# Performance work log

Hardware: AMD Instinct MI355X
Metric: run time of the kernel (lower is better)

The kernel has to match this reference:

```python
import jax, jax.numpy as jnp
import numpy as np

N, E, G = 100000, 3200000, 5000
EPS = 1e-5
HEADS, HC = 8, 16


def setup_inputs() -> dict:
    key = jax.random.key(0)
    k = jax.random.split(key, 12)

    def lin(kk, fi, fo):
        return (jax.random.normal(kk, (fi, fo), jnp.float32) / np.sqrt(fi)).astype(jnp.float32)

    return {
        "x": jax.random.normal(k[0], (N, 20), jnp.float32),
        "edge_index": jax.random.randint(k[1], (2, E), 0, N, dtype=jnp.int32),
        "batch": jnp.sort(jax.random.randint(k[2], (N,), 0, G, dtype=jnp.int32)),
        "W1": lin(k[3], 20, 64), "b1": jnp.zeros((64,), jnp.float32),
        "g1": jnp.ones((64,), jnp.float32), "be1": jnp.zeros((64,), jnp.float32),
        "W2": lin(k[4], 64, 32), "b2": jnp.zeros((32,), jnp.float32),
        "g2": jnp.ones((32,), jnp.float32), "be2": jnp.zeros((32,), jnp.float32),
        "W3": lin(k[5], 32, 16), "b3": jnp.zeros((16,), jnp.float32),
        "g3": jnp.ones((16,), jnp.float32), "be3": jnp.zeros((16,), jnp.float32),
        "Wg": lin(k[6], 16, HEADS * HC),
        "att_src": jax.random.normal(k[7], (HEADS, HC), jnp.float32) * 0.1,
        "att_dst": jax.random.normal(k[8], (HEADS, HC), jnp.float32) * 0.1,
        "bg": jnp.zeros((HC,), jnp.float32),
        "Wf": lin(k[9], 16, 3), "bf": jnp.zeros((3,), jnp.float32),
    }


def reference(x, edge_index, batch,
              W1, b1, g1, be1, W2, b2, g2, be2, W3, b3, g3, be3,
              Wg, att_src, att_dst, bg, Wf, bf):
    src, dst = edge_index[0], edge_index[1]
    loop = jnp.arange(N, dtype=src.dtype)
    src_sl = jnp.concatenate([src, loop])  # self-loops (GCN + GAT add_self_loops)
    dst_sl = jnp.concatenate([dst, loop])

    # GCN symmetric normalization D^-1/2 (A+I) D^-1/2
    deg = jax.ops.segment_sum(jnp.ones_like(src_sl, dtype=jnp.float32), dst_sl, N)
    dinv = jnp.where(deg > 0, 1.0 / jnp.sqrt(deg), 0.0)
    norm = (dinv[src_sl] * dinv[dst_sl])[:, None]  # [E+N, 1]

    def gcn(h, W, b):
        h = h @ W
        return jax.ops.segment_sum(h[src_sl] * norm, dst_sl, N) + b

    def bn_relu(h, g, b):  # BatchNorm1d (train-mode batch stats) + ReLU
        mu = h.mean(0)
        var = ((h - mu) ** 2).mean(0)
        return jax.nn.relu(g * (h - mu) * jax.lax.rsqrt(var + EPS) + b)

    h = bn_relu(gcn(x, W1, b1), g1, be1)   # dropout = identity (eval)
    h = bn_relu(gcn(h, W2, b2), g2, be2)
    h = bn_relu(gcn(h, W3, b3), g3, be3)

    # GATConv: heads=8, concat=False (mean over heads), eval -> no dropout
    xg = (h @ Wg).reshape(N, HEADS, HC)
    a_src = (xg * att_src).sum(-1)  # [N, H]
    a_dst = (xg * att_dst).sum(-1)
    logit = jax.nn.leaky_relu(a_src[src_sl] + a_dst[dst_sl], 0.2)  # [E+N, H]
    m = jax.ops.segment_max(logit, dst_sl, N)          # segment softmax over dst
    e = jnp.exp(logit - m[dst_sl])
    s = jax.ops.segment_sum(e, dst_sl, N)
    alpha = e / s[dst_sl]
    agg = jax.ops.segment_sum(xg[src_sl] * alpha[:, :, None], dst_sl, N)  # [N,H,C]
    hg = agg.mean(1) + bg  # [N, 16]

    pooled = jax.ops.segment_sum(hg, batch, G)  # global_add_pool -> [G, 16]
    return pooled @ Wf + bf  # [G, 3]
```

## Files before the change

### kernel.cpp

```cpp
#include <hip/hip_runtime.h>
#include <hip/hip_fp16.h>

constexpr int NN = 100000;
constexpr int EE = 3200000;
constexpr int GG = 5000;
constexpr float BNEPS = 1e-5f;

constexpr int BINS = 128;
constexpr int NPB = (NN + BINS - 1) / BINS;
constexpr int BCHUNK = 8192;
constexpr int NBCH = (EE + BCHUNK - 1) / BCHUNK;
constexpr int BINCAP2 = 96;
constexpr int BINREG = 27648;
constexpr int LCAP = 26624;
constexpr int CTR_STRIDE = 32;

typedef int int4v __attribute__((ext_vector_type(4)));


__global__ __launch_bounds__(1024) void bin_edges(const int* __restrict__ ei,
                                                  uint2* __restrict__ pairs,
                                                  int* __restrict__ binCur) {
    __shared__ int bcnt[BINS];
    __shared__ int bbase[BINS];
    __shared__ uint2 buf[BINS][BINCAP2];
    const int t = threadIdx.x;
    const int lane = t & 63, wv = t >> 6;
    for (int ch = blockIdx.x; ch < NBCH; ch += gridDim.x) {
        for (int k = t; k < BINS; k += 1024) bcnt[k] = 0;
        __syncthreads();
        const int qbase = ch * (BCHUNK / 4);
#pragma unroll
        for (int rep = 0; rep < 2; ++rep) {
            const int q = qbase + rep * 1024 + t;
            if (q < EE / 4) {
                int4v d = __builtin_nontemporal_load((const int4v*)(ei + EE) + q);
                int4v s = __builtin_nontemporal_load((const int4v*)ei + q);
                int dd[4] = {d.x, d.y, d.z, d.w};
                int ss[4] = {s.x, s.y, s.z, s.w};
#pragma unroll
                for (int k = 0; k < 4; ++k) {
                    int o = dd[k] / NPB;
                    int p = atomicAdd(&bcnt[o], 1);
                    if (p < BINCAP2) {
                        buf[o][p] = make_uint2((unsigned)dd[k], (unsigned)ss[k]);
                    } else {
                        int gp = atomicAdd(&binCur[o * CTR_STRIDE], 1);
                        pairs[(size_t)o * BINREG + gp] =
                            make_uint2((unsigned)dd[k], (unsigned)ss[k]);
                    }
                }
            }
        }
        __syncthreads();
        if (t < BINS) {
            int c = bcnt[t] < BINCAP2 ? bcnt[t] : BINCAP2;
            bbase[t] = atomicAdd(&binCur[t * CTR_STRIDE], c);
            bcnt[t] = c;
        }
        __syncthreads();
        for (int o = wv; o < BINS; o += 16) {
            const int c = bcnt[o];
            const size_t base = (size_t)o * BINREG + bbase[o];
            for (int k = lane; k < c; k += 64) pairs[base + k] = buf[o][k];
        }
        __syncthreads();
    }
}


__global__ void bin_base(const int* __restrict__ binCur, int* __restrict__ binBase) {
    __shared__ int s[BINS];
    const int t = threadIdx.x;
    const int v = binCur[t * CTR_STRIDE];
    s[t] = v;
    __syncthreads();
    for (int off = 1; off < BINS; off <<= 1) {
        int add = (t >= off) ? s[t - off] : 0;
        __syncthreads();
        s[t] += add;
        __syncthreads();
    }
    binBase[t] = s[t] - v;
}


__global__ __launch_bounds__(1024) void scatter_lds(const uint2* __restrict__ pairs,
                                                    const int* __restrict__ binCur,
                                                    const int* __restrict__ binBase,
                                                    int* __restrict__ rowptr,
                                                    float* __restrict__ dinv,
                                                    int* __restrict__ colA) {
    __shared__ int scnt[NPB];
    __shared__ int sscan[1024];
    __shared__ int lbuf[LCAP];
    const int b = blockIdx.x;
    const int t = threadIdx.x;
    const int lo = b * NPB;
    const int hi = (lo + NPB < NN) ? lo + NPB : NN;
    const int nb = hi - lo;
    const int tot = binCur[b * CTR_STRIDE];
    const int base = binBase[b];
    const uint2* p = pairs + (size_t)b * BINREG;
    for (int k = t; k < nb; k += 1024) scnt[k] = 0;
    __syncthreads();
    for (int q = t; q < tot; q += 1024) atomicAdd(&scnt[p[q].x - lo], 1);
    __syncthreads();
    const int myc = (t < nb) ? scnt[t] : 0;
    sscan[t] = myc;
    __syncthreads();
    for (int off = 1; off < 1024; off <<= 1) {
        int add = (t >= off) ? sscan[t - off] : 0;
        __syncthreads();
        sscan[t] += add;
        __syncthreads();
    }
    const int excl = sscan[t] - myc;
    if (t < nb) {
        rowptr[lo + t] = base + excl;
        dinv[lo + t] = rsqrtf((float)(myc + 1));
        scnt[t] = excl;
    }
    if (b == BINS - 1 && t == 0) rowptr[NN] = base + tot;
    __syncthreads();
    for (int q = t; q < tot; q += 1024) {
        uint2 e = p[q];
        int pos = atomicAdd(&scnt[e.x - lo], 1);
        if (pos < LCAP) lbuf[pos] = (int)e.y;
        else colA[base + pos] = (int)e.y;
    }
    __syncthreads();
    const int m = tot < LCAP ? tot : LCAP;
    for (int k = t; k < m; k += 1024) colA[base + k] = lbuf[k];
}


__global__ void scale_x(const float* __restrict__ x, const float* __restrict__ dinv,
                        __half* __restrict__ xsc) {
    int idx = blockIdx.x * blockDim.x + threadIdx.x;
    if (idx < NN * 20) {
        int n = idx / 20;
        xsc[idx] = __float2half(x[idx] * dinv[n]);
    }
}


template <int FIN, int FOUT, bool AFFINE, bool SCALED, bool STATS>
__global__ void gemm_k(const float* __restrict__ hin,
                       const float* __restrict__ sumsIn, const float* __restrict__ ssqIn,
                       const float* __restrict__ g, const float* __restrict__ be,
                       const float* __restrict__ W, const float* __restrict__ dinv,
                       const float* __restrict__ bias,
                       float* __restrict__ outF, __half* __restrict__ outH,
                       float* __restrict__ sumsOut, float* __restrict__ ssqOut) {
    constexpr int NB = 256 / FOUT;
    __shared__ float Wl[FIN * FOUT];
    __shared__ float rows[NB][FIN];
    __shared__ float aa[AFFINE ? FIN : 1], bb[AFFINE ? FIN : 1];
    const int t = threadIdx.x;
    if constexpr (AFFINE) {
        if (t < FIN) {
            float mu = sumsIn[t] / (float)NN;
            float var = ssqIn[t] / (float)NN - mu * mu;
            float a = g[t] * rsqrtf(var + BNEPS);
            aa[t] = a;
            bb[t] = be[t] - mu * a;
        }
    }
    for (int i = t; i < FIN * FOUT; i += 256) Wl[i] = W[i];
    const int c = t % FOUT, s = t / FOUT;
    const int ngrp = (NN + NB - 1) / NB;
    float sAcc = 0.f, qAcc = 0.f;
    for (int grp = blockIdx.x; grp < ngrp; grp += gridDim.x) {
        __syncthreads();
        for (int i = t; i < NB * FIN; i += 256) {
            int sn = i / FIN, k = i % FIN;
            int n2 = grp * NB + sn;
            float v = 0.f;
            if (n2 < NN) {
                v = hin[(size_t)n2 * FIN + k];
                if constexpr (AFFINE) {
                    v = aa[k] * v + bb[k];
                    v = v > 0.f ? v : 0.f;
                }
            }
            rows[sn][k] = v;
        }
        __syncthreads();
        int node = grp * NB + s;
        if (node < NN) {
            float acc = 0.f;
#pragma unroll
            for (int k = 0; k < FIN; ++k) acc += rows[s][k] * Wl[k * FOUT + c];
            if constexpr (SCALED) {
                outH[(size_t)node * FOUT + c] = __float2half(acc * dinv[node]);
            } else {
                float val = acc + bias[c];
                outF[(size_t)node * FOUT + c] = val;
                if constexpr (STATS) { sAcc += val; qAcc += val * val; }
            }
        }
    }
    if constexpr (STATS) {
        __shared__ float ls[FOUT], lq[FOUT];
        __syncthreads();
        if (t < FOUT) { ls[t] = 0.f; lq[t] = 0.f; }
        __syncthreads();
        atomicAdd(&ls[c], sAcc);
        atomicAdd(&lq[c], qAcc);
        __syncthreads();
        if (t < FOUT) { atomicAdd(&sumsOut[t], ls[t]); atomicAdd(&ssqOut[t], lq[t]); }
    }
}


template <int H2, int OUTF, bool STATS>
__global__ void agg_half(const __half2* __restrict__ src, const int* __restrict__ rowptr,
                         const int* __restrict__ colA, const float* __restrict__ dinv,
                         const float* __restrict__ bias, float* __restrict__ out,
                         float* __restrict__ sumsOut, float* __restrict__ ssqOut) {
    constexpr int SUB = 64 / H2;
    const int lane = threadIdx.x & 63;
    const int wid = (blockIdx.x * blockDim.x + threadIdx.x) >> 6;
    const int totalWaves = (gridDim.x * blockDim.x) >> 6;
    const int f = lane % H2;
    const int sub = lane / H2;
    const int stride = totalWaves * SUB;
    float bx = 0.f, by = 0.f;
    if (bias != nullptr) {
        bx = bias[2 * f];
        by = (2 * f + 1 < OUTF) ? bias[2 * f + 1] : 0.f;
    }
    const int i0 = (sub < SUB) ? wid * SUB + sub : NN;
    float sx = 0.f, qx = 0.f, sy = 0.f, qy = 0.f;
    for (int i = i0; i < NN; i += stride) {
        const int r0 = rowptr[i], r1 = rowptr[i + 1];
        float2 acc = __half22float2(src[(size_t)i * H2 + f]);
        float2 acc2 = {0.f, 0.f};
        int e = r0;
        for (; e + 3 < r1; e += 4) {
            int j0 = colA[e], j1 = colA[e + 1], j2 = colA[e + 2], j3 = colA[e + 3];
            float2 v0 = __half22float2(src[(size_t)j0 * H2 + f]);
            float2 v1 = __half22float2(src[(size_t)j1 * H2 + f]);
            float2 v2 = __half22float2(src[(size_t)j2 * H2 + f]);
            float2 v3 = __half22float2(src[(size_t)j3 * H2 + f]);
            acc.x += v0.x + v1.x;
            acc.y += v0.y + v1.y;
            acc2.x += v2.x + v3.x;
            acc2.y += v2.y + v3.y;
        }
        for (; e < r1; ++e) {
            float2 v = __half22float2(src[(size_t)colA[e] * H2 + f]);
            acc.x += v.x; acc.y += v.y;
        }
        acc.x += acc2.x; acc.y += acc2.y;
        const float d = dinv[i];
        float vx = d * acc.x + bx;
        out[(size_t)i * OUTF + 2 * f] = vx;
        if constexpr (STATS) { sx += vx; qx += vx * vx; }
        if (2 * f + 1 < OUTF) {
            float vy = d * acc.y + by;
            out[(size_t)i * OUTF + 2 * f + 1] = vy;
            if constexpr (STATS) { sy += vy; qy += vy * vy; }
        }
    }
    if constexpr (STATS) {
        __shared__ float ls[OUTF], lq[OUTF];
        const int t = threadIdx.x;
        if (t < OUTF) { ls[t] = 0.f; lq[t] = 0.f; }
        __syncthreads();
        atomicAdd(&ls[2 * f], sx);
        atomicAdd(&lq[2 * f], qx);
        if (2 * f + 1 < OUTF) {
            atomicAdd(&ls[2 * f + 1], sy);
            atomicAdd(&lq[2 * f + 1], qy);
        }
        __syncthreads();
        if (t < OUTF) { atomicAdd(&sumsOut[t], ls[t]); atomicAdd(&ssqOut[t], lq[t]); }
    }
}


__global__ void gat_mats(const float* __restrict__ Wg, const float* __restrict__ att_src,
                         const float* __restrict__ att_dst, const float* __restrict__ Wf,
                         const float* __restrict__ bg, float* __restrict__ Psrc,
                         float* __restrict__ Pdst, float* __restrict__ M,
                         float* __restrict__ bgW) {
    int t = threadIdx.x;
    if (t < 128) {
        int k = t >> 3, h = t & 7;
        float s = 0.f, d = 0.f;
        for (int c = 0; c < 16; ++c) {
            float wv = Wg[k * 128 + h * 16 + c];
            s += wv * att_src[h * 16 + c];
            d += wv * att_dst[h * 16 + c];
        }
        Psrc[k * 8 + h] = s;
        Pdst[k * 8 + h] = d;
    } else if (t < 512) {
        int m = t - 128;
        if (m < 384) {
            int hk = m / 3, j = m - hk * 3;
            int H = hk >> 4, k = hk & 15;
            float s = 0.f;
            for (int c = 0; c < 16; ++c) s += Wg[k * 128 + H * 16 + c] * Wf[c * 3 + j];
            M[hk * 3 + j] = 0.125f * s;
        }
    } else if (t < 515) {
        int j = t - 512;
        float s = 0.f;
        for (int c = 0; c < 16; ++c) s += bg[c] * Wf[c * 3 + j];
        bgW[j] = s;
    }
}


__global__ void gat_pre2(const float* __restrict__ h3,
                         const float* __restrict__ sums3, const float* __restrict__ ssq3,
                         const float* __restrict__ g3, const float* __restrict__ be3,
                         const float* __restrict__ Psrc, const float* __restrict__ Pdst,
                         float4* __restrict__ zas, float* __restrict__ adst) {
    __shared__ float Ps[128], Pd[128], aa[16], bb[16];
    int t = threadIdx.x;
    if (t < 128) { Ps[t] = Psrc[t]; Pd[t] = Pdst[t]; }
    if (t < 16) {
        float mu = sums3[t] / (float)NN;
        float var = ssq3[t] / (float)NN - mu * mu;
        float a = g3[t] * rsqrtf(var + BNEPS);
        aa[t] = a;
        bb[t] = be3[t] - mu * a;
    }
    __syncthreads();
    int n = blockIdx.x * blockDim.x + t;
    if (n >= NN) return;
    float zv[16];
#pragma unroll
    for (int k = 0; k < 16; ++k) {
        float v = h3[(size_t)n * 16 + k];
        v = aa[k] * v + bb[k];
        zv[k] = v > 0.f ? v : 0.f;
    }
    __half2 zh[8];
#pragma unroll
    for (int k = 0; k < 8; ++k) zh[k] = __floats2half2_rn(zv[2 * k], zv[2 * k + 1]);
    float as[8], ad[8];
#pragma unroll
    for (int h = 0; h < 8; ++h) { as[h] = 0.f; ad[h] = 0.f; }
#pragma unroll
    for (int k = 0; k < 16; ++k) {
        float zk = zv[k];
#pragma unroll
        for (int h = 0; h < 8; ++h) {
            as[h] += zk * Ps[k * 8 + h];
            ad[h] += zk * Pd[k * 8 + h];
        }
    }
    float4* zrow = zas + (size_t)n * 4;
    zrow[0] = ((float4*)zh)[0];
    zrow[1] = ((float4*)zh)[1];
    zrow[2] = make_float4(as[0], as[1], as[2], as[3]);
    zrow[3] = make_float4(as[4], as[5], as[6], as[7]);
    float4* d4 = (float4*)(adst + (size_t)n * 8);
    d4[0] = make_float4(ad[0], ad[1], ad[2], ad[3]);
    d4[1] = make_float4(ad[4], ad[5], ad[6], ad[7]);
}


__device__ __forceinline__ float leaky02(float x) { return x > 0.f ? x : 0.2f * x; }

__global__ void gat_agg6(const float4* __restrict__ zas, const float* __restrict__ adst,
                         const int* __restrict__ rowptr, const int* __restrict__ colA,
                         __half* __restrict__ Sn) {
    const int lane = threadIdx.x & 63;
    const int ls = lane & 7;
    const int q = ls & 3;
    const int hh = ls >> 2;
    const int grp = lane >> 3;
    const int gb = lane & 56;
    const int wid = (blockIdx.x * blockDim.x + threadIdx.x) >> 6;
    const int totalWaves = (gridDim.x * blockDim.x) >> 6;
    const int stride = totalWaves * 8;
    const char* zb = (const char*)zas;
    for (int i = wid * 8 + grp; i < NN; i += stride) {
        const int r0 = rowptr[i], r1 = rowptr[i + 1];
        const float adv = adst[(size_t)i * 8 + ls];
        float acc[4][4];
        float wsum[4];
#pragma unroll
        for (int h = 0; h < 4; ++h) {
            wsum[h] = 0.f;
#pragma unroll
            for (int k = 0; k < 4; ++k) acc[h][k] = 0.f;
        }
        auto body = [&](int j) {
            const char* row = zb + (size_t)j * 64;
            const float av = *(const float*)(row + 32 + ls * 4);
            const float2 zr = *(const float2*)(row + q * 8);
            const __half2* zp = (const __half2*)&zr;
            const float2 f0 = __half22float2(zp[0]), f1 = __half22float2(zp[1]);
            const float zf[4] = {f0.x, f0.y, f1.x, f1.y};
            const float w = __expf(leaky02(av + adv));
            float wq[4];
#pragma unroll
            for (int h = 0; h < 4; ++h) wq[h] = __shfl(w, gb + hh * 4 + h);
#pragma unroll
            for (int h = 0; h < 4; ++h) {
                wsum[h] += wq[h];
#pragma unroll
                for (int k = 0; k < 4; ++k) acc[h][k] += wq[h] * zf[k];
            }
        };
        body(i);
        for (int e = r0; e < r1; ++e) body(colA[e]);
#pragma unroll
        for (int h = 0; h < 4; ++h) {
            const float inv = 1.f / wsum[h];
            __half2 o[2];
            o[0] = __floats2half2_rn(acc[h][0] * inv, acc[h][1] * inv);
            o[1] = __floats2half2_rn(acc[h][2] * inv, acc[h][3] * inv);
            *(float2*)(Sn + (size_t)i * 128 + (hh * 4 + h) * 16 + q * 4) = *(float2*)o;
        }
    }
}


__global__ void graph_bounds(const int* __restrict__ batch, int* __restrict__ gstart) {
    int n = blockIdx.x * blockDim.x + threadIdx.x;
    if (n < NN) {
        int bn = batch[n];
        int bp = (n == 0) ? -1 : batch[n - 1];
        for (int g = bp + 1; g <= bn; ++g) gstart[g] = n;
        if (n == NN - 1)
            for (int g = bn + 1; g <= GG; ++g) gstart[g] = NN;
    }
}


__global__ void pool_final(const __half2* __restrict__ Sn2, const int* __restrict__ gstart,
                           const float* __restrict__ M, const float* __restrict__ bgW,
                           const float* __restrict__ bf, float* __restrict__ out) {
    const int lane = threadIdx.x & 63;
    const int g = (blockIdx.x * blockDim.x + threadIdx.x) >> 6;
    if (g >= GG) return;
    const int n0 = gstart[g], n1 = gstart[g + 1];
    float2 s = {0.f, 0.f};
    for (int n = n0; n < n1; ++n) {
        float2 v = __half22float2(Sn2[(size_t)n * 64 + lane]);
        s.x += v.x;
        s.y += v.y;
    }
    float o[3];
#pragma unroll
    for (int j = 0; j < 3; ++j)
        o[j] = s.x * M[(2 * lane) * 3 + j] + s.y * M[(2 * lane + 1) * 3 + j];
#pragma unroll
    for (int off = 1; off < 64; off <<= 1) {
#pragma unroll
        for (int j = 0; j < 3; ++j) o[j] += __shfl_xor(o[j], off);
    }
    if (lane == 0) {
        float cnt = (float)(n1 - n0);
#pragma unroll
        for (int j = 0; j < 3; ++j) out[g * 3 + j] = o[j] + cnt * bgW[j] + bf[j];
    }
}


extern "C" void kernel_launch(void* const* d_in, const int* in_sizes, int n_in,
                              void* d_out, int out_size, void* d_ws, size_t ws_size,
                              hipStream_t stream) {
    const float* x = (const float*)d_in[0];
    const int* ei = (const int*)d_in[1];
    const int* batch = (const int*)d_in[2];
    const float* W1 = (const float*)d_in[3];  const float* b1 = (const float*)d_in[4];
    const float* g1 = (const float*)d_in[5];  const float* be1 = (const float*)d_in[6];
    const float* W2 = (const float*)d_in[7];  const float* b2 = (const float*)d_in[8];
    const float* g2 = (const float*)d_in[9];  const float* be2 = (const float*)d_in[10];
    const float* W3 = (const float*)d_in[11]; const float* b3 = (const float*)d_in[12];
    const float* g3 = (const float*)d_in[13]; const float* be3 = (const float*)d_in[14];
    const float* Wg = (const float*)d_in[15];
    const float* att_src = (const float*)d_in[16];
    const float* att_dst = (const float*)d_in[17];
    const float* bg = (const float*)d_in[18];
    const float* Wf = (const float*)d_in[19];
    const float* bf = (const float*)d_in[20];
    float* out = (float*)d_out;

    char* w = (char*)d_ws;
    auto alloc = [&](size_t bytes) -> char* {
        char* p = w;
        w += (bytes + 255) & ~(size_t)255;
        return p;
    };
    int* binCur = (int*)alloc((size_t)BINS * CTR_STRIDE * 4);
    float* sums1 = (float*)alloc(64 * 4); float* ssq1 = (float*)alloc(64 * 4);
    float* sums2 = (float*)alloc(32 * 4); float* ssq2 = (float*)alloc(32 * 4);
    float* sums3 = (float*)alloc(16 * 4); float* ssq3 = (float*)alloc(16 * 4);
    size_t zeroBytes = (size_t)(w - (char*)d_ws);
    int* binBase = (int*)alloc((size_t)BINS * 4);
    float* Psrc = (float*)alloc(128 * 4);
    float* Pdst = (float*)alloc(128 * 4);
    float* Mm = (float*)alloc(384 * 4);
    float* bgW = (float*)alloc(3 * 4);
    int* gstart = (int*)alloc((size_t)(GG + 1) * 4);
    int* rowptr = (int*)alloc((size_t)(NN + 1) * 4);
    int* colA = (int*)alloc((size_t)EE * 4);
    float* dinv = (float*)alloc((size_t)NN * 4);
    char* A = alloc((size_t)NN * 64 * 4);
    char* B = alloc((size_t)NN * 64 * 4);

    uint2*  pairs = (uint2*)A;
    __half* xsc  = (__half*)B;
    float*  aggx = (float*)(B + (size_t)NN * 32 * 2);
    float*  h1   = (float*)A;
    __half* hs2  = (__half*)B;
    float*  h2   = (float*)(B + (size_t)NN * 32 * 2);
    __half* hs3  = (__half*)A;
    float*  h3   = (float*)(A + (size_t)NN * 16 * 2);
    char*   zas  = A + (size_t)NN * 96;
    float*  adst = (float*)(A + (size_t)NN * 160);
    __half* Sn   = (__half*)B;

    hipMemsetAsync(d_ws, 0, zeroBytes, stream);

    bin_edges<<<256, 1024, 0, stream>>>(ei, pairs, binCur);
    bin_base<<<1, BINS, 0, stream>>>(binCur, binBase);
    scatter_lds<<<BINS, 1024, 0, stream>>>(pairs, binCur, binBase, rowptr, dinv, colA);
    gat_mats<<<1, 1024, 0, stream>>>(Wg, att_src, att_dst, Wf, bg, Psrc, Pdst, Mm, bgW);
    graph_bounds<<<(NN + 255) / 256, 256, 0, stream>>>(batch, gstart);

    scale_x<<<(NN * 20 + 255) / 256, 256, 0, stream>>>(x, dinv, xsc);
    agg_half<10, 20, false><<<2048, 256, 0, stream>>>((const __half2*)xsc, rowptr, colA, dinv,
                                                      nullptr, aggx, nullptr, nullptr);
    gemm_k<20, 64, false, false, true><<<2048, 256, 0, stream>>>(
        aggx, nullptr, nullptr, nullptr, nullptr, W1, dinv, b1, h1, nullptr, sums1, ssq1);

    gemm_k<64, 32, true, true, false><<<2048, 256, 0, stream>>>(
        h1, sums1, ssq1, g1, be1, W2, dinv, nullptr, nullptr, hs2, nullptr, nullptr);
    agg_half<16, 32, true><<<2048, 256, 0, stream>>>((const __half2*)hs2, rowptr, colA, dinv,
                                                     b2, h2, sums2, ssq2);

    gemm_k<32, 16, true, true, false><<<2048, 256, 0, stream>>>(
        h2, sums2, ssq2, g2, be2, W3, dinv, nullptr, nullptr, hs3, nullptr, nullptr);
    agg_half<8, 16, true><<<2048, 256, 0, stream>>>((const __half2*)hs3, rowptr, colA, dinv,
                                                    b3, h3, sums3, ssq3);

    gat_pre2<<<(NN + 255) / 256, 256, 0, stream>>>(h3, sums3, ssq3, g3, be3, Psrc, Pdst,
                                                   (float4*)zas, adst);
    gat_agg6<<<3200, 256, 0, stream>>>((const float4*)zas, adst, rowptr, colA, Sn);
    pool_final<<<(GG * 64 + 255) / 256, 256, 0, stream>>>((const __half2*)Sn, gstart, Mm, bgW,
                                                          bf, out);
}
```

Before: 494.3 us.

## Fuse GAT aggregation with pooling and final projection via atomics; software-pipeline gathers

Folds the final 128x3 projection and global add pooling into the GAT aggregation kernel. Each node's normalized per-head output is multiplied by the projection matrix held in LDS, reduced across lanes, and atomically added into the graph output, which a new init kernel pre-fills with the bias terms. This removes the fp16 Sn intermediate write and read and the separate pool kernel. The neighbor loop is also software-pipelined to prefetch two neighbor rows ahead, and the adst load is marked nontemporal. The cost is float atomics contending on per-graph outputs, which also makes the summation order nondeterministic.

```diff
diff --git a/kernel.cpp b/kernel.cpp
--- a/kernel.cpp
+++ b/kernel.cpp
@@ -368,9 +368,13 @@
 
 __device__ __forceinline__ float leaky02(float x) { return x > 0.f ? x : 0.2f * x; }
 
-__global__ void gat_agg6(const float4* __restrict__ zas, const float* __restrict__ adst,
+__global__ void gat_agg7(const float4* __restrict__ zas, const float* __restrict__ adst,
                          const int* __restrict__ rowptr, const int* __restrict__ colA,
-                         __half* __restrict__ Sn) {
+                         const int* __restrict__ batch, const float* __restrict__ Mg,
+                         float* __restrict__ out) {
+    __shared__ float Ml[384];
+    for (int k = threadIdx.x; k < 384; k += 256) Ml[k] = Mg[k];
+    __syncthreads();
     const int lane = threadIdx.x & 63;
     const int ls = lane & 7;
     const int q = ls & 3;
@@ -383,7 +387,7 @@
     const char* zb = (const char*)zas;
     for (int i = wid * 8 + grp; i < NN; i += stride) {
         const int r0 = rowptr[i], r1 = rowptr[i + 1];
-        const float adv = adst[(size_t)i * 8 + ls];
+        const float adv = __builtin_nontemporal_load(adst + (size_t)i * 8 + ls);
         float acc[4][4];
         float wsum[4];
 #pragma unroll
@@ -392,14 +396,11 @@
 #pragma unroll
             for (int k = 0; k < 4; ++k) acc[h][k] = 0.f;
         }
-        auto body = [&](int j) {
-            const char* row = zb + (size_t)j * 64;
-            const float av = *(const float*)(row + 32 + ls * 4);
-            const float2 zr = *(const float2*)(row + q * 8);
+        auto compute = [&](float av, float2 zr, bool val) {
             const __half2* zp = (const __half2*)&zr;
             const float2 f0 = __half22float2(zp[0]), f1 = __half22float2(zp[1]);
             const float zf[4] = {f0.x, f0.y, f1.x, f1.y};
-            const float w = __expf(leaky02(av + adv));
+            const float w = val ? __expf(leaky02(av + adv)) : 0.f;
             float wq[4];
 #pragma unroll
             for (int h = 0; h < 4; ++h) wq[h] = __shfl(w, gb + hh * 4 + h);
@@ -410,15 +411,56 @@
                 for (int k = 0; k < 4; ++k) acc[h][k] += wq[h] * zf[k];
             }
         };
-        body(i);
-        for (int e = r0; e < r1; ++e) body(colA[e]);
+        int e = r0;
+        int jA = i, jB = i;
+        bool vB = false;
+        if (e < r1) { jB = colA[e]; ++e; vB = true; }
+        const char* rowA = zb + (size_t)jA * 64;
+        const char* rowB = zb + (size_t)jB * 64;
+        float avA = *(const float*)(rowA + 32 + ls * 4);
+        float2 zA = *(const float2*)(rowA + q * 8);
+        float avB = *(const float*)(rowB + 32 + ls * 4);
+        float2 zB = *(const float2*)(rowB + q * 8);
+        while (true) {
+            int jA2 = i, jB2 = i;
+            bool vA2 = false, vB2 = false;
+            if (e < r1) { jA2 = colA[e]; ++e; vA2 = true; }
+            if (e < r1) { jB2 = colA[e]; ++e; vB2 = true; }
+            const char* rA2 = zb + (size_t)jA2 * 64;
+            const char* rB2 = zb + (size_t)jB2 * 64;
+            float avA2 = *(const float*)(rA2 + 32 + ls * 4);
+            float2 zA2 = *(const float2*)(rA2 + q * 8);
+            float avB2 = *(const float*)(rB2 + 32 + ls * 4);
+            float2 zB2 = *(const float2*)(rB2 + q * 8);
+            compute(avA, zA, true);
+            compute(avB, zB, vB);
+            if (!vA2) break;
+            avA = avA2; zA = zA2; avB = avB2; zB = zB2; vB = vB2;
+        }
+        float o0 = 0.f, o1 = 0.f, o2 = 0.f;
 #pragma unroll
         for (int h = 0; h < 4; ++h) {
             const float inv = 1.f / wsum[h];
-            __half2 o[2];
-            o[0] = __floats2half2_rn(acc[h][0] * inv, acc[h][1] * inv);
-            o[1] = __floats2half2_rn(acc[h][2] * inv, acc[h][3] * inv);
-            *(float2*)(Sn + (size_t)i * 128 + (hh * 4 + h) * 16 + q * 4) = *(float2*)o;
+            const int hk0 = (hh * 4 + h) * 16 + q * 4;
+#pragma unroll
+            for (int k = 0; k < 4; ++k) {
+                const float v = acc[h][k] * inv;
+                const float* m = &Ml[(hk0 + k) * 3];
+                o0 += v * m[0];
+                o1 += v * m[1];
+                o2 += v * m[2];
+            }
+        }
+#pragma unroll
+        for (int off = 1; off < 8; off <<= 1) {
+            o0 += __shfl_xor(o0, off);
+            o1 += __shfl_xor(o1, off);
+            o2 += __shfl_xor(o2, off);
+        }
+        const int g = batch[i];
+        if (ls < 3) {
+            const float ov = (ls == 0) ? o0 : (ls == 1) ? o1 : o2;
+            atomicAdd(&out[g * 3 + ls], ov);
         }
     }
 }
@@ -436,32 +478,13 @@
 }
 
 
-__global__ void pool_final(const __half2* __restrict__ Sn2, const int* __restrict__ gstart,
-                           const float* __restrict__ M, const float* __restrict__ bgW,
-                           const float* __restrict__ bf, float* __restrict__ out) {
-    const int lane = threadIdx.x & 63;
-    const int g = (blockIdx.x * blockDim.x + threadIdx.x) >> 6;
-    if (g >= GG) return;
-    const int n0 = gstart[g], n1 = gstart[g + 1];
-    float2 s = {0.f, 0.f};
-    for (int n = n0; n < n1; ++n) {
-        float2 v = __half22float2(Sn2[(size_t)n * 64 + lane]);
-        s.x += v.x;
-        s.y += v.y;
-    }
-    float o[3];
-#pragma unroll
-    for (int j = 0; j < 3; ++j)
-        o[j] = s.x * M[(2 * lane) * 3 + j] + s.y * M[(2 * lane + 1) * 3 + j];
-#pragma unroll
-    for (int off = 1; off < 64; off <<= 1) {
-#pragma unroll
-        for (int j = 0; j < 3; ++j) o[j] += __shfl_xor(o[j], off);
-    }
-    if (lane == 0) {
-        float cnt = (float)(n1 - n0);
-#pragma unroll
-        for (int j = 0; j < 3; ++j) out[g * 3 + j] = o[j] + cnt * bgW[j] + bf[j];
+__global__ void pool_init(const int* __restrict__ gstart, const float* __restrict__ bgW,
+                          const float* __restrict__ bf, float* __restrict__ out) {
+    int g = blockIdx.x * blockDim.x + threadIdx.x;
+    if (g < GG) {
+        float cnt = (float)(gstart[g + 1] - gstart[g]);
+#pragma unroll
+        for (int j = 0; j < 3; ++j) out[g * 3 + j] = cnt * bgW[j] + bf[j];
     }
 }
 
@@ -519,7 +542,6 @@
     float*  h3   = (float*)(A + (size_t)NN * 16 * 2);
     char*   zas  = A + (size_t)NN * 96;
     float*  adst = (float*)(A + (size_t)NN * 160);
-    __half* Sn   = (__half*)B;
 
     hipMemsetAsync(d_ws, 0, zeroBytes, stream);
 
@@ -528,6 +550,7 @@
     scatter_lds<<<BINS, 1024, 0, stream>>>(pairs, binCur, binBase, rowptr, dinv, colA);
     gat_mats<<<1, 1024, 0, stream>>>(Wg, att_src, att_dst, Wf, bg, Psrc, Pdst, Mm, bgW);
     graph_bounds<<<(NN + 255) / 256, 256, 0, stream>>>(batch, gstart);
+    pool_init<<<(GG + 255) / 256, 256, 0, stream>>>(gstart, bgW, bf, out);
 
     scale_x<<<(NN * 20 + 255) / 256, 256, 0, stream>>>(x, dinv, xsc);
     agg_half<10, 20, false><<<2048, 256, 0, stream>>>((const __half2*)xsc, rowptr, colA, dinv,
@@ -547,7 +570,5 @@
 
     gat_pre2<<<(NN + 255) / 256, 256, 0, stream>>>(h3, sums3, ssq3, g3, be3, Psrc, Pdst,
                                                    (float4*)zas, adst);
-    gat_agg6<<<3200, 256, 0, stream>>>((const float4*)zas, adst, rowptr, colA, Sn);
-    pool_final<<<(GG * 64 + 255) / 256, 256, 0, stream>>>((const __half2*)Sn, gstart, Mm, bgW,
-                                                          bf, out);
-}
+    gat_agg7<<<3200, 256, 0, stream>>>((const float4*)zas, adst, rowptr, colA, batch, Mm, out);
+}
```

Result: faster. 468.9 us (-5.1%).
